# Optimization experiments

Measured on AMD Instinct MI355X. Metric: run time of the kernel, lower is better.

Reference implementation:

```python
import jax, jax.numpy as jnp
import numpy as np

N = 100000   # total nodes (batched graphs)
E = 800000   # random edges (self-loops appended -> E+N total)
G = 2000     # number of graphs in batch
H = 4        # heads per GAT layer
D = 64       # hidden_size (per-head out dim)
IN = 64      # in_feats
EXTRA = 8    # extra graph-level feats
HID = H * D  # 256


def setup_inputs() -> dict:
    key = jax.random.key(0)
    ks = jax.random.split(key, 24)
    s = 0.5  # init std used in the torch module
    feats_node = jax.random.normal(ks[0], (N, IN), jnp.float32)
    feats_graph = jax.random.normal(ks[1], (G, EXTRA), jnp.float32)
    # edges + self loops (DGL GATConv requires no zero-in-degree nodes)
    src = jnp.concatenate([jax.random.randint(ks[2], (E,), 0, N), jnp.arange(N)])
    dst = jnp.concatenate([jax.random.randint(ks[3], (E,), 0, N), jnp.arange(N)])
    node_gid = jnp.sort(jax.random.randint(ks[4], (N,), 0, G))
    # GAT layer 1
    W1 = jax.random.normal(ks[5], (IN, HID), jnp.float32) * s
    al1 = jax.random.normal(ks[6], (H, D), jnp.float32) * s
    ar1 = jax.random.normal(ks[7], (H, D), jnp.float32) * s
    b1 = jnp.zeros((HID,), jnp.float32)
    # GAT layer 2
    W2 = jax.random.normal(ks[8], (HID, HID), jnp.float32) * s
    al2 = jax.random.normal(ks[9], (H, D), jnp.float32) * s
    ar2 = jax.random.normal(ks[10], (H, D), jnp.float32) * s
    b2 = jnp.zeros((HID,), jnp.float32)
    # WeightedAverage readout score
    Ws = jax.random.normal(ks[11], (HID, 1), jnp.float32) * s
    bs = jnp.zeros((1,), jnp.float32)
    # MLP: 264 -> 128 -> 64 -> 1 with SELU
    Wm1 = jax.random.normal(ks[12], (HID + EXTRA, 2 * D), jnp.float32) * s
    bm1 = jnp.zeros((2 * D,), jnp.float32)
    Wm2 = jax.random.normal(ks[13], (2 * D, D), jnp.float32) * s
    bm2 = jnp.zeros((D,), jnp.float32)
    Wm3 = jax.random.normal(ks[14], (D, 1), jnp.float32) * s
    bm3 = jnp.zeros((1,), jnp.float32)
    return dict(feats_node=feats_node, feats_graph=feats_graph,
                W1=W1, al1=al1, ar1=ar1, b1=b1,
                W2=W2, al2=al2, ar2=ar2, b2=b2,
                Ws=Ws, bs=bs, Wm1=Wm1, bm1=bm1, Wm2=Wm2, bm2=bm2,
                Wm3=Wm3, bm3=bm3,
                src=src, dst=dst, node_gid=node_gid)


def gat_layer(x, W, al, ar, b, src, dst):
    # DGL GATConv: fc -> per-node attn projections -> edge leaky_relu ->
    # edge softmax over incoming edges -> weighted scatter-sum -> +bias
    f = (x @ W).reshape(N, H, D)                       # [N,H,D]
    el = jnp.einsum('nhd,hd->nh', f, al)               # [N,H]
    er = jnp.einsum('nhd,hd->nh', f, ar)               # [N,H]
    e = jax.nn.leaky_relu(el[src] + er[dst], 0.2)      # [E',H]
    m = jax.ops.segment_max(e, dst, num_segments=N)    # per-dst max
    e = jnp.exp(e - m[dst])
    denom = jax.ops.segment_sum(e, dst, num_segments=N)
    alpha = e / denom[dst]                             # edge softmax [E',H]
    out = jax.ops.segment_sum(alpha[:, :, None] * f[src], dst, num_segments=N)
    return out.reshape(N, HID) + b


def reference(feats_node, feats_graph, W1, al1, ar1, b1, W2, al2, ar2, b2,
              Ws, bs, Wm1, bm1, Wm2, bm2, Wm3, bm3, src, dst, node_gid):
    x = jax.nn.relu(gat_layer(feats_node, W1, al1, ar1, b1, src, dst))
    x = jax.nn.relu(gat_layer(x, W2, al2, ar2, b2, src, dst))
    # weighted-average readout per graph: sum(w*x)/sum(w)
    w = jax.nn.sigmoid(x @ Ws + bs)                    # [N,1]
    num = jax.ops.segment_sum(w * x, node_gid, num_segments=G)
    den = jax.ops.segment_sum(w, node_gid, num_segments=G)
    emb = num / jnp.where(den == 0, 1.0, den)          # [G,HID]
    h = jnp.concatenate([emb, feats_graph], axis=1)    # [G,HID+EXTRA]
    h = jax.nn.selu(h @ Wm1 + bm1)
    h = jax.nn.selu(h @ Wm2 + bm2)
    return h @ Wm3 + bm3                               # [G,1]
```

## Files before the change

kernel.cpp:

```cpp
#include <hip/hip_runtime.h>
#include <hip/hip_bf16.h>
#include <math.h>

#define NN     100000
#define GG     2000
#define HH     4
#define DD     64
#define HID    256
#define INF_   64
#define EXTRA  8

typedef unsigned short u16;
typedef __attribute__((ext_vector_type(8))) short bf16x8;
typedef __attribute__((ext_vector_type(4))) float f32x4;

__device__ __forceinline__ u16 f2bf(float f) {
    unsigned u = __float_as_uint(f);
    return (u16)((u + 0x7fffu + ((u >> 16) & 1u)) >> 16);
}
__device__ __forceinline__ float bf2f(u16 v) {
    return __uint_as_float(((unsigned)v) << 16);
}

__global__ __launch_bounds__(256) void wsplit_kernel(
    const float* __restrict__ W, u16* __restrict__ hi, u16* __restrict__ lo,
    int K, int lgK)
{
    int idx = blockIdx.x * 256 + threadIdx.x;
    if (idx >= 256 * K) return;
    int n = idx >> lgK, k = idx & (K - 1);
    float w = W[k * HID + n];
    u16 h = f2bf(w);
    hi[idx] = h;
    lo[idx] = f2bf(w - bf2f(h));
}

__global__ __launch_bounds__(256) void walprep_kernel(
    const float* __restrict__ W1, const float* __restrict__ al,
    const float* __restrict__ ar, float* __restrict__ wal, float* __restrict__ war)
{
    int tid = threadIdx.x;
    int d = tid >> 2, h = tid & 3;
    const float* wrow = W1 + d * HID + h * DD;
    const float* av = al + h * DD;
    const float* bv = ar + h * DD;
    float s1 = 0.f, s2 = 0.f;
    for (int c = 0; c < DD; ++c) { s1 += wrow[c] * av[c]; s2 += wrow[c] * bv[c]; }
    wal[d * 4 + h] = s1;
    war[d * 4 + h] = s2;
}

__global__ __launch_bounds__(256) void elr1_kernel(
    const float* __restrict__ feats, const float* __restrict__ wal,
    const float* __restrict__ war, float* __restrict__ el, float* __restrict__ er)
{
    int idx = blockIdx.x * 256 + threadIdx.x;
    if (idx >= NN * HH) return;
    int n = idx >> 2, h = idx & 3;
    const float* f = feats + (size_t)n * INF_;
    float s1 = 0.f, s2 = 0.f;
    #pragma unroll 4
    for (int d = 0; d < INF_; d += 4) {
        float4 fv = *reinterpret_cast<const float4*>(f + d);
        s1 += fv.x * wal[(d + 0) * 4 + h] + fv.y * wal[(d + 1) * 4 + h]
            + fv.z * wal[(d + 2) * 4 + h] + fv.w * wal[(d + 3) * 4 + h];
        s2 += fv.x * war[(d + 0) * 4 + h] + fv.y * war[(d + 1) * 4 + h]
            + fv.z * war[(d + 2) * 4 + h] + fv.w * war[(d + 3) * 4 + h];
    }
    el[idx] = s1;
    er[idx] = s2;
}

__global__ __launch_bounds__(256) void aggregate_feats_kernel(
    const float* __restrict__ feats, const float* __restrict__ w,
    const float* __restrict__ invden, const int* __restrict__ rowptr,
    const int* __restrict__ colsrc, u16* __restrict__ Yh, u16* __restrict__ Yl)
{
    int t = blockIdx.x * 4 + (threadIdx.x >> 6);
    int lane = threadIdx.x & 63;
    if (t >= NN) return;
    int beg = rowptr[t], end = rowptr[t + 1];
    float a0 = 0.f, a1 = 0.f, a2 = 0.f, a3 = 0.f;
    float b0 = 0.f, b1 = 0.f, b2 = 0.f, b3 = 0.f;
    int i = beg;
    for (; i + 1 < end; i += 2) {
        int s0 = colsrc[i], s1 = colsrc[i + 1];
        float4 w0 = *reinterpret_cast<const float4*>(w + (size_t)i * 4);
        float4 w1 = *reinterpret_cast<const float4*>(w + (size_t)(i + 1) * 4);
        float f0 = feats[(size_t)s0 * INF_ + lane];
        float f1 = feats[(size_t)s1 * INF_ + lane];
        a0 += w0.x * f0; a1 += w0.y * f0; a2 += w0.z * f0; a3 += w0.w * f0;
        b0 += w1.x * f1; b1 += w1.y * f1; b2 += w1.z * f1; b3 += w1.w * f1;
    }
    if (i < end) {
        int s0 = colsrc[i];
        float4 w0 = *reinterpret_cast<const float4*>(w + (size_t)i * 4);
        float f0 = feats[(size_t)s0 * INF_ + lane];
        a0 += w0.x * f0; a1 += w0.y * f0; a2 += w0.z * f0; a3 += w0.w * f0;
    }
    float4 inv = *reinterpret_cast<const float4*>(invden + (size_t)t * 4);
    float y0 = (a0 + b0) * inv.x;
    float y1 = (a1 + b1) * inv.y;
    float y2 = (a2 + b2) * inv.z;
    float y3 = (a3 + b3) * inv.w;
    u16* yh = Yh + (size_t)t * HID;
    u16* yl = Yl + (size_t)t * HID;
    u16 h0 = f2bf(y0), h1 = f2bf(y1), h2 = f2bf(y2), h3 = f2bf(y3);
    yh[lane] = h0;        yl[lane] = f2bf(y0 - bf2f(h0));
    yh[64 + lane] = h1;   yl[64 + lane] = f2bf(y1 - bf2f(h1));
    yh[128 + lane] = h2;  yl[128 + lane] = f2bf(y2 - bf2f(h2));
    yh[192 + lane] = h3;  yl[192 + lane] = f2bf(y3 - bf2f(h3));
}

__global__ __launch_bounds__(256) void gemm_head_kernel(
    const u16* __restrict__ Yh, const u16* __restrict__ Yl,
    const u16* __restrict__ BThi, const u16* __restrict__ BTlo,
    const float* __restrict__ bias,
    u16* __restrict__ Xh, u16* __restrict__ Xl, int M)
{
    __shared__ __align__(16) u16 Ah[128 * 64];
    __shared__ __align__(16) u16 Al[128 * 64];
    __shared__ __align__(16) u16 Bh[64 * 64];
    __shared__ __align__(16) u16 Bl[64 * 64];
    const int tid  = threadIdx.x;
    const int wave = tid >> 6, lane = tid & 63;
    const int quad = lane >> 4, l15 = lane & 15;
    const int wy = wave >> 1, wx = wave & 1;
    const int head = blockIdx.y;
    const int r0 = blockIdx.x * 128;
    const int cb = head * DD;

    {
        int row = tid >> 1, half = tid & 1;
        int gr = min(r0 + row, M - 1);
        size_t goff = (size_t)gr * HID + cb;
        #pragma unroll
        for (int m = 0; m < 4; ++m) {
            int c = half * 4 + m;
            int cs = c ^ (row & 7);
            *reinterpret_cast<bf16x8*>(&Ah[row * 64 + cs * 8]) =
                *reinterpret_cast<const bf16x8*>(Yh + goff + c * 8);
            *reinterpret_cast<bf16x8*>(&Al[row * 64 + cs * 8]) =
                *reinterpret_cast<const bf16x8*>(Yl + goff + c * 8);
        }
        int d = tid & 63, seg = tid >> 6;
        size_t boff = (size_t)(head * DD + d) * 64;
        #pragma unroll
        for (int m = 0; m < 2; ++m) {
            int c = seg * 2 + m;
            int cs = c ^ (d & 7);
            *reinterpret_cast<bf16x8*>(&Bh[d * 64 + cs * 8]) =
                *reinterpret_cast<const bf16x8*>(BThi + boff + c * 8);
            *reinterpret_cast<bf16x8*>(&Bl[d * 64 + cs * 8]) =
                *reinterpret_cast<const bf16x8*>(BTlo + boff + c * 8);
        }
    }
    __syncthreads();

    f32x4 acc[4][2];
    #pragma unroll
    for (int i = 0; i < 4; ++i)
        #pragma unroll
        for (int j = 0; j < 2; ++j)
            acc[i][j] = (f32x4){0.f, 0.f, 0.f, 0.f};

    #pragma unroll
    for (int k0 = 0; k0 < 64; k0 += 32) {
        bf16x8 afh[4], afl[4], bfh[2], bfl[2];
        #pragma unroll
        for (int i = 0; i < 4; ++i) {
            int Ra = wy * 64 + i * 16 + l15;
            int c = (k0 >> 3) + quad;
            int cs = c ^ (Ra & 7);
            afh[i] = *reinterpret_cast<const bf16x8*>(&Ah[Ra * 64 + cs * 8]);
            afl[i] = *reinterpret_cast<const bf16x8*>(&Al[Ra * 64 + cs * 8]);
        }
        #pragma unroll
        for (int j = 0; j < 2; ++j) {
            int Rb = wx * 32 + j * 16 + l15;
            int c = (k0 >> 3) + quad;
            int cs = c ^ (Rb & 7);
            bfh[j] = *reinterpret_cast<const bf16x8*>(&Bh[Rb * 64 + cs * 8]);
            bfl[j] = *reinterpret_cast<const bf16x8*>(&Bl[Rb * 64 + cs * 8]);
        }
        #pragma unroll
        for (int i = 0; i < 4; ++i)
            #pragma unroll
            for (int j = 0; j < 2; ++j) {
                acc[i][j] = __builtin_amdgcn_mfma_f32_16x16x32_bf16(afh[i], bfh[j], acc[i][j], 0, 0, 0);
                acc[i][j] = __builtin_amdgcn_mfma_f32_16x16x32_bf16(afl[i], bfh[j], acc[i][j], 0, 0, 0);
                acc[i][j] = __builtin_amdgcn_mfma_f32_16x16x32_bf16(afh[i], bfl[j], acc[i][j], 0, 0, 0);
            }
    }

    float bv[2];
    #pragma unroll
    for (int j = 0; j < 2; ++j) bv[j] = bias[cb + wx * 32 + j * 16 + l15];
    #pragma unroll
    for (int i = 0; i < 4; ++i)
        #pragma unroll
        for (int rr = 0; rr < 4; ++rr) {
            int grow = r0 + wy * 64 + i * 16 + quad * 4 + rr;
            if (grow < M) {
                size_t base = (size_t)grow * HID + cb + wx * 32 + l15;
                #pragma unroll
                for (int j = 0; j < 2; ++j) {
                    float x = fmaxf(acc[i][j][rr] + bv[j], 0.f);
                    u16 h = f2bf(x);
                    Xh[base + j * 16] = h;
                    Xl[base + j * 16] = f2bf(x - bf2f(h));
                }
            }
        }
}

__global__ __launch_bounds__(256) void mfma_gemm_kernel(
    const u16* __restrict__ Ahg, const u16* __restrict__ Alg,
    const u16* __restrict__ BThi, const u16* __restrict__ BTlo,
    u16* __restrict__ Cb,
    const float* __restrict__ al, const float* __restrict__ ar,
    float* __restrict__ el, float* __restrict__ er, int M, int K)
{
    __shared__ __align__(16) u16 Ah[128 * 32];
    __shared__ __align__(16) u16 Al[128 * 32];
    __shared__ __align__(16) u16 Bh[128 * 32];
    __shared__ __align__(16) u16 Bl[128 * 32];
    const int tid  = threadIdx.x;
    const int wave = tid >> 6, lane = tid & 63;
    const int quad = lane >> 4, l15 = lane & 15;
    const int wy = wave >> 1, wx = wave & 1;
    const int r0 = blockIdx.x * 128, c0 = blockIdx.y * 128;
    const int sr = tid >> 2, sseg = tid & 3;

    f32x4 acc[4][4];
    #pragma unroll
    for (int i = 0; i < 4; ++i)
        #pragma unroll
        for (int j = 0; j < 4; ++j)
            acc[i][j] = (f32x4){0.f, 0.f, 0.f, 0.f};

    for (int k0 = 0; k0 < K; k0 += 32) {
        #pragma unroll
        for (int half = 0; half < 2; ++half) {
            int r = sr + half * 64;
            int cs = (sseg ^ (r & 3)) * 8;
            int gr = min(r0 + r, M - 1);
            size_t aoff = (size_t)gr * K + k0 + sseg * 8;
            *reinterpret_cast<bf16x8*>(&Ah[r * 32 + cs]) =
                *reinterpret_cast<const bf16x8*>(Ahg + aoff);
            *reinterpret_cast<bf16x8*>(&Al[r * 32 + cs]) =
                *reinterpret_cast<const bf16x8*>(Alg + aoff);
            int gc = c0 + r;
            size_t boff = (size_t)gc * K + k0 + sseg * 8;
            *reinterpret_cast<bf16x8*>(&Bh[r * 32 + cs]) =
                *reinterpret_cast<const bf16x8*>(BThi + boff);
            *reinterpret_cast<bf16x8*>(&Bl[r * 32 + cs]) =
                *reinterpret_cast<const bf16x8*>(BTlo + boff);
        }
        __syncthreads();
        bf16x8 afh[4], afl[4], bfh[4], bfl[4];
        #pragma unroll
        for (int i = 0; i < 4; ++i) {
            int Ra = wy * 64 + i * 16 + l15;
            int off = Ra * 32 + (quad ^ (Ra & 3)) * 8;
            afh[i] = *reinterpret_cast<const bf16x8*>(&Ah[off]);
            afl[i] = *reinterpret_cast<const bf16x8*>(&Al[off]);
        }
        #pragma unroll
        for (int j = 0; j < 4; ++j) {
            int Rb = wx * 64 + j * 16 + l15;
            int off = Rb * 32 + (quad ^ (Rb & 3)) * 8;
            bfh[j] = *reinterpret_cast<const bf16x8*>(&Bh[off]);
            bfl[j] = *reinterpret_cast<const bf16x8*>(&Bl[off]);
        }
        #pragma unroll
        for (int i = 0; i < 4; ++i)
            #pragma unroll
            for (int j = 0; j < 4; ++j) {
                acc[i][j] = __builtin_amdgcn_mfma_f32_16x16x32_bf16(afh[i], bfh[j], acc[i][j], 0, 0, 0);
                acc[i][j] = __builtin_amdgcn_mfma_f32_16x16x32_bf16(afl[i], bfh[j], acc[i][j], 0, 0, 0);
                acc[i][j] = __builtin_amdgcn_mfma_f32_16x16x32_bf16(afh[i], bfl[j], acc[i][j], 0, 0, 0);
            }
        __syncthreads();
    }

    #pragma unroll
    for (int i = 0; i < 4; ++i)
        #pragma unroll
        for (int rr = 0; rr < 4; ++rr) {
            int grow = r0 + wy * 64 + i * 16 + quad * 4 + rr;
            if (grow < M) {
                u16* crow = Cb + (size_t)grow * HID + c0 + wx * 64 + l15;
                #pragma unroll
                for (int j = 0; j < 4; ++j) crow[j * 16] = f2bf(acc[i][j][rr]);
            }
        }

    const int h = blockIdx.y * 2 + wx;
    float alf[4], arf[4];
    #pragma unroll
    for (int j = 0; j < 4; ++j) {
        alf[j] = al[h * DD + j * 16 + l15];
        arf[j] = ar[h * DD + j * 16 + l15];
    }
    #pragma unroll
    for (int i = 0; i < 4; ++i)
        #pragma unroll
        for (int rr = 0; rr < 4; ++rr) {
            float sl = acc[i][0][rr] * alf[0] + acc[i][1][rr] * alf[1]
                     + acc[i][2][rr] * alf[2] + acc[i][3][rr] * alf[3];
            float sr_ = acc[i][0][rr] * arf[0] + acc[i][1][rr] * arf[1]
                      + acc[i][2][rr] * arf[2] + acc[i][3][rr] * arf[3];
            #pragma unroll
            for (int off = 1; off < 16; off <<= 1) {
                sl  += __shfl_xor(sl, off, 64);
                sr_ += __shfl_xor(sr_, off, 64);
            }
            if (l15 == 0) {
                int grow = r0 + wy * 64 + i * 16 + quad * 4 + rr;
                if (grow < M) {
                    el[grow * 4 + h] = sl;
                    er[grow * 4 + h] = sr_;
                }
            }
        }
}

__device__ __forceinline__ float leaky02(float x) { return x > 0.f ? x : 0.2f * x; }

__global__ __launch_bounds__(256) void edge_softmax_kernel(
    const float* __restrict__ el, const float* __restrict__ er,
    const int* __restrict__ rowptr, const int* __restrict__ colsrc,
    float* __restrict__ w, float* __restrict__ invden)
{
    int idx = blockIdx.x * 256 + threadIdx.x;
    if (idx >= NN * HH) return;
    int t = idx >> 2, h = idx & 3;
    int beg = rowptr[t], end = rowptr[t + 1];
    float ert = er[idx];
    float m = -1e30f;
    for (int i = beg; i < end; ++i) {
        int s = colsrc[i];
        m = fmaxf(m, leaky02(el[s * 4 + h] + ert));
    }
    float den = 0.f;
    for (int i = beg; i < end; ++i) {
        int s = colsrc[i];
        float v = expf(leaky02(el[s * 4 + h] + ert) - m);
        w[(size_t)i * 4 + h] = v;
        den += v;
    }
    invden[idx] = 1.f / den;
}

__global__ __launch_bounds__(256) void aggregate_bf16_kernel(
    const u16* __restrict__ F, const float* __restrict__ w,
    const float* __restrict__ invden, const int* __restrict__ rowptr,
    const int* __restrict__ colsrc, const float* __restrict__ bias,
    u16* __restrict__ out)
{
    int t = blockIdx.x * 4 + (threadIdx.x >> 6);
    int lane = threadIdx.x & 63;
    if (t >= NN) return;
    int beg = rowptr[t], end = rowptr[t + 1];
    const int h = lane >> 4;
    float4 acc0 = make_float4(0.f, 0.f, 0.f, 0.f);
    float4 acc1 = make_float4(0.f, 0.f, 0.f, 0.f);
    int i = beg;
    for (; i + 1 < end; i += 2) {
        int s0 = colsrc[i], s1 = colsrc[i + 1];
        float w0 = w[(size_t)i * 4 + h];
        float w1 = w[(size_t)(i + 1) * 4 + h];
        ushort4 f0 = *reinterpret_cast<const ushort4*>(F + (size_t)s0 * HID + 4 * lane);
        ushort4 f1 = *reinterpret_cast<const ushort4*>(F + (size_t)s1 * HID + 4 * lane);
        acc0.x += w0 * bf2f(f0.x); acc0.y += w0 * bf2f(f0.y);
        acc0.z += w0 * bf2f(f0.z); acc0.w += w0 * bf2f(f0.w);
        acc1.x += w1 * bf2f(f1.x); acc1.y += w1 * bf2f(f1.y);
        acc1.z += w1 * bf2f(f1.z); acc1.w += w1 * bf2f(f1.w);
    }
    if (i < end) {
        int s0 = colsrc[i];
        float w0 = w[(size_t)i * 4 + h];
        ushort4 f0 = *reinterpret_cast<const ushort4*>(F + (size_t)s0 * HID + 4 * lane);
        acc0.x += w0 * bf2f(f0.x); acc0.y += w0 * bf2f(f0.y);
        acc0.z += w0 * bf2f(f0.z); acc0.w += w0 * bf2f(f0.w);
    }
    float inv = invden[t * 4 + h];
    float4 bv = *reinterpret_cast<const float4*>(bias + 4 * lane);
    ushort4 r;
    r.x = f2bf(fmaxf((acc0.x + acc1.x) * inv + bv.x, 0.f));
    r.y = f2bf(fmaxf((acc0.y + acc1.y) * inv + bv.y, 0.f));
    r.z = f2bf(fmaxf((acc0.z + acc1.z) * inv + bv.z, 0.f));
    r.w = f2bf(fmaxf((acc0.w + acc1.w) * inv + bv.w, 0.f));
    *reinterpret_cast<ushort4*>(out + (size_t)t * HID + 4 * lane) = r;
}

__global__ __launch_bounds__(256) void readout_kernel(
    const u16* __restrict__ X, const float* __restrict__ Ws,
    const float* __restrict__ bs, const int* __restrict__ gptr,
    float* __restrict__ emb)
{
    int g = blockIdx.x * 4 + (threadIdx.x >> 6);
    int lane = threadIdx.x & 63;
    if (g >= GG) return;
    int beg = gptr[g], end = gptr[g + 1];
    float4 wv = *reinterpret_cast<const float4*>(Ws + 4 * lane);
    float b = bs[0];
    float4 acc = make_float4(0.f, 0.f, 0.f, 0.f);
    float wsum = 0.f;
    for (int n = beg; n < end; ++n) {
        ushort4 xv = *reinterpret_cast<const ushort4*>(X + (size_t)n * HID + 4 * lane);
        float x0 = bf2f(xv.x), x1 = bf2f(xv.y), x2 = bf2f(xv.z), x3 = bf2f(xv.w);
        float p = x0 * wv.x + x1 * wv.y + x2 * wv.z + x3 * wv.w;
        #pragma unroll
        for (int off = 32; off; off >>= 1) p += __shfl_xor(p, off, 64);
        float w = 1.f / (1.f + expf(-(p + b)));
        wsum += w;
        acc.x += w * x0; acc.y += w * x1; acc.z += w * x2; acc.w += w * x3;
    }
    float inv = (wsum == 0.f) ? 1.f : wsum;
    float4 e;
    e.x = acc.x / inv; e.y = acc.y / inv; e.z = acc.z / inv; e.w = acc.w / inv;
    *reinterpret_cast<float4*>(emb + (size_t)g * HID + 4 * lane) = e;
}

__device__ __forceinline__ float selu_f(float x)
{
    const float scale = 1.0507009873554805f, alpha = 1.6732632423543772f;
    return scale * (x > 0.f ? x : alpha * expm1f(x));
}

__global__ __launch_bounds__(128) void mlp_kernel(
    const float* __restrict__ emb, const float* __restrict__ fg,
    const float* __restrict__ Wm1, const float* __restrict__ bm1,
    const float* __restrict__ Wm2, const float* __restrict__ bm2,
    const float* __restrict__ Wm3, const float* __restrict__ bm3,
    float* __restrict__ out)
{
    int g = blockIdx.x;
    __shared__ float h[HID + EXTRA];
    __shared__ float h1[128];
    __shared__ float h2[64];
    int tid = threadIdx.x;
    h[tid] = emb[(size_t)g * HID + tid];
    h[128 + tid] = emb[(size_t)g * HID + 128 + tid];
    if (tid < EXTRA) h[HID + tid] = fg[(size_t)g * EXTRA + tid];
    __syncthreads();
    float acc = bm1[tid];
    for (int i = 0; i < HID + EXTRA; ++i) acc += h[i] * Wm1[i * 128 + tid];
    h1[tid] = selu_f(acc);
    __syncthreads();
    if (tid < 64) {
        float acc2 = bm2[tid];
        for (int i = 0; i < 128; ++i) acc2 += h1[i] * Wm2[i * 64 + tid];
        h2[tid] = selu_f(acc2);
    }
    __syncthreads();
    if (tid < 64) {
        float p = h2[tid] * Wm3[tid];
        #pragma unroll
        for (int off = 32; off; off >>= 1) p += __shfl_xor(p, off, 64);
        if (tid == 0) out[g] = p + bm3[0];
    }
}

__global__ void count_dst_kernel(const int* __restrict__ dst, int* __restrict__ cnt, int E)
{
    int e = blockIdx.x * 256 + threadIdx.x;
    if (e < E) atomicAdd(&cnt[dst[e]], 1);
}
__global__ void count_gid_kernel(const int* __restrict__ gid, int* __restrict__ cnt, int n)
{
    int i = blockIdx.x * 256 + threadIdx.x;
    if (i < n) atomicAdd(&cnt[gid[i]], 1);
}
__global__ void fill_csr_kernel(const int* __restrict__ src, const int* __restrict__ dst,
                                int* __restrict__ cursor, int* __restrict__ colsrc, int E)
{
    int e = blockIdx.x * 256 + threadIdx.x;
    if (e < E) {
        int p = atomicAdd(&cursor[dst[e]], 1);
        colsrc[p] = src[e];
    }
}

__global__ __launch_bounds__(256) void scan_blocks_kernel(
    const int* __restrict__ in, int n, int* __restrict__ out, int* __restrict__ partials)
{
    __shared__ int lds[256];
    int tid = threadIdx.x;
    int base = blockIdx.x * 1024 + tid * 4;
    int v0 = (base + 0 < n) ? in[base + 0] : 0;
    int v1 = (base + 1 < n) ? in[base + 1] : 0;
    int v2 = (base + 2 < n) ? in[base + 2] : 0;
    int v3 = (base + 3 < n) ? in[base + 3] : 0;
    int s = v0 + v1 + v2 + v3;
    lds[tid] = s;
    __syncthreads();
    for (int off = 1; off < 256; off <<= 1) {
        int t = (tid >= off) ? lds[tid - off] : 0;
        __syncthreads();
        lds[tid] += t;
        __syncthreads();
    }
    int excl = lds[tid] - s;
    if (base + 0 < n) out[base + 0] = excl;
    if (base + 1 < n) out[base + 1] = excl + v0;
    if (base + 2 < n) out[base + 2] = excl + v0 + v1;
    if (base + 3 < n) out[base + 3] = excl + v0 + v1 + v2;
    if (tid == 255) partials[blockIdx.x] = lds[255];
}

__global__ __launch_bounds__(256) void scan_partials_kernel(int* partials, int nb)
{
    __shared__ int lds[256];
    int tid = threadIdx.x;
    int v = (tid < nb) ? partials[tid] : 0;
    lds[tid] = v;
    __syncthreads();
    for (int off = 1; off < 256; off <<= 1) {
        int t = (tid >= off) ? lds[tid - off] : 0;
        __syncthreads();
        lds[tid] += t;
        __syncthreads();
    }
    int excl = lds[tid] - v;
    if (tid < nb) partials[tid] = excl;
}

__global__ void add_offsets_kernel(int* __restrict__ out, const int* __restrict__ partials, int n)
{
    int i = blockIdx.x * 256 + threadIdx.x;
    if (i < n) out[i] += partials[i >> 10];
}

extern "C" void kernel_launch(void* const* d_in, const int* in_sizes, int n_in,
                              void* d_out, int out_size, void* d_ws, size_t ws_size,
                              hipStream_t stream)
{
    const float* feats_node  = (const float*)d_in[0];
    const float* feats_graph = (const float*)d_in[1];
    const float* W1  = (const float*)d_in[2];
    const float* al1 = (const float*)d_in[3];
    const float* ar1 = (const float*)d_in[4];
    const float* b1  = (const float*)d_in[5];
    const float* W2  = (const float*)d_in[6];
    const float* al2 = (const float*)d_in[7];
    const float* ar2 = (const float*)d_in[8];
    const float* b2  = (const float*)d_in[9];
    const float* Ws  = (const float*)d_in[10];
    const float* bs  = (const float*)d_in[11];
    const float* Wm1 = (const float*)d_in[12];
    const float* bm1 = (const float*)d_in[13];
    const float* Wm2 = (const float*)d_in[14];
    const float* bm2 = (const float*)d_in[15];
    const float* Wm3 = (const float*)d_in[16];
    const float* bm3 = (const float*)d_in[17];
    const int* src = (const int*)d_in[18];
    const int* dst = (const int*)d_in[19];
    const int* gid = (const int*)d_in[20];
    float* out = (float*)d_out;
    const int E = in_sizes[18];

    char* p = (char*)d_ws;
    auto alloc = [&](size_t bytes) {
        char* r = p;
        p += (bytes + 255) & ~(size_t)255;
        return r;
    };
    u16*   Yh     = (u16*)alloc((size_t)NN * HID * 2);
    u16*   Yl     = (u16*)alloc((size_t)NN * HID * 2);
    u16*   Xh     = (u16*)alloc((size_t)NN * HID * 2);
    u16*   Xl     = (u16*)alloc((size_t)NN * HID * 2);
    float* el     = (float*)alloc((size_t)NN * HH * 4);
    float* er     = (float*)alloc((size_t)NN * HH * 4);
    float* wbuf   = (float*)alloc((size_t)E * HH * 4);
    float* invden = (float*)alloc((size_t)NN * HH * 4);
    int*   cnt    = (int*)alloc((size_t)(NN + 1) * 4);
    int*   rowptr = (int*)alloc((size_t)(NN + 1) * 4);
    int*   colsrc = (int*)alloc((size_t)E * 4);
    int*   gcnt   = (int*)alloc((size_t)(GG + 1) * 4);
    int*   gptr   = (int*)alloc((size_t)(GG + 1) * 4);
    int*   parts  = (int*)alloc(1024 * 4);
    float* emb    = (float*)alloc((size_t)GG * HID * 4);
    u16*   BT1h   = (u16*)alloc((size_t)HID * INF_ * 2);
    u16*   BT1l   = (u16*)alloc((size_t)HID * INF_ * 2);
    u16*   BT2h   = (u16*)alloc((size_t)HID * HID * 2);
    u16*   BT2l   = (u16*)alloc((size_t)HID * HID * 2);
    float* wal1   = (float*)alloc(INF_ * HH * 4);
    float* war1   = (float*)alloc(INF_ * HH * 4);
    u16*   Fbf2   = Yh;
    u16*   Xbf2   = Xh;

    hipMemsetAsync(cnt, 0, (size_t)(NN + 1) * 4, stream);
    count_dst_kernel<<<(E + 255) / 256, 256, 0, stream>>>(dst, cnt, E);
    {
        int n = NN + 1, nb = (n + 1023) / 1024;
        scan_blocks_kernel<<<nb, 256, 0, stream>>>(cnt, n, rowptr, parts);
        scan_partials_kernel<<<1, 256, 0, stream>>>(parts, nb);
        add_offsets_kernel<<<(n + 255) / 256, 256, 0, stream>>>(rowptr, parts, n);
    }
    hipMemcpyAsync(cnt, rowptr, (size_t)(NN + 1) * 4, hipMemcpyDeviceToDevice, stream);
    fill_csr_kernel<<<(E + 255) / 256, 256, 0, stream>>>(src, dst, cnt, colsrc, E);

    hipMemsetAsync(gcnt, 0, (size_t)(GG + 1) * 4, stream);
    count_gid_kernel<<<(NN + 255) / 256, 256, 0, stream>>>(gid, gcnt, NN);
    {
        int n = GG + 1, nb = (n + 1023) / 1024;
        scan_blocks_kernel<<<nb, 256, 0, stream>>>(gcnt, n, gptr, parts);
        scan_partials_kernel<<<1, 256, 0, stream>>>(parts, nb);
        add_offsets_kernel<<<(n + 255) / 256, 256, 0, stream>>>(gptr, parts, n);
    }

    wsplit_kernel<<<(HID * INF_ + 255) / 256, 256, 0, stream>>>(W1, BT1h, BT1l, INF_, 6);
    wsplit_kernel<<<(HID * HID + 255) / 256, 256, 0, stream>>>(W2, BT2h, BT2l, HID, 8);
    walprep_kernel<<<1, 256, 0, stream>>>(W1, al1, ar1, wal1, war1);

    const int nh_blocks = (NN * HH + 255) / 256;

    elr1_kernel<<<nh_blocks, 256, 0, stream>>>(feats_node, wal1, war1, el, er);
    edge_softmax_kernel<<<nh_blocks, 256, 0, stream>>>(el, er, rowptr, colsrc, wbuf, invden);
    aggregate_feats_kernel<<<(NN + 3) / 4, 256, 0, stream>>>(feats_node, wbuf, invden,
                                                             rowptr, colsrc, Yh, Yl);
    {
        dim3 hgrid((NN + 127) / 128, HH);
        gemm_head_kernel<<<hgrid, 256, 0, stream>>>(Yh, Yl, BT1h, BT1l, b1, Xh, Xl, NN);
    }

    dim3 ggrid((NN + 127) / 128, HID / 128);
    mfma_gemm_kernel<<<ggrid, 256, 0, stream>>>(
        Xh, Xl, BT2h, BT2l, Fbf2, al2, ar2, el, er, NN, HID);
    edge_softmax_kernel<<<nh_blocks, 256, 0, stream>>>(el, er, rowptr, colsrc, wbuf, invden);
    aggregate_bf16_kernel<<<(NN + 3) / 4, 256, 0, stream>>>(Fbf2, wbuf, invden, rowptr, colsrc,
                                                            b2, Xbf2);

    readout_kernel<<<(GG + 3) / 4, 256, 0, stream>>>(Xbf2, Ws, bs, gptr, emb);
    mlp_kernel<<<GG, 128, 0, stream>>>(emb, feats_graph, Wm1, bm1, Wm2, bm2, Wm3, bm3, out);
}
```

Measured before the change: 630.5 us.

## Fuse layer-2 edge softmax into aggregation, fix LDS swizzle, compute graph ranges directly

Layer-2 edge softmax now runs inside the aggregation kernel, which recomputes the max, exponentials and denominator per node. This removes one kernel launch and the round-trip of per-edge weights through global memory, at the cost of redundant exp work across lanes and an extra pass over the edges for the max. The GEMM LDS swizzle now XORs with (row>>1)&3 to reduce bank conflicts. Graph pointer ranges are computed directly from the sorted gid array instead of atomic counting plus a multi-kernel scan.

```diff
diff --git a/kernel.cpp b/kernel.cpp
--- a/kernel.cpp
+++ b/kernel.cpp
@@ -69,6 +69,33 @@
     }
     el[idx] = s1;
     er[idx] = s2;
+}
+
+__device__ __forceinline__ float leaky02(float x) { return x > 0.f ? x : 0.2f * x; }
+
+__global__ __launch_bounds__(256) void edge_softmax_kernel(
+    const float* __restrict__ el, const float* __restrict__ er,
+    const int* __restrict__ rowptr, const int* __restrict__ colsrc,
+    float* __restrict__ w, float* __restrict__ invden)
+{
+    int idx = blockIdx.x * 256 + threadIdx.x;
+    if (idx >= NN * HH) return;
+    int t = idx >> 2, h = idx & 3;
+    int beg = rowptr[t], end = rowptr[t + 1];
+    float ert = er[idx];
+    float m = -1e30f;
+    for (int i = beg; i < end; ++i) {
+        int s = colsrc[i];
+        m = fmaxf(m, leaky02(el[s * 4 + h] + ert));
+    }
+    float den = 0.f;
+    for (int i = beg; i < end; ++i) {
+        int s = colsrc[i];
+        float v = expf(leaky02(el[s * 4 + h] + ert) - m);
+        w[(size_t)i * 4 + h] = v;
+        den += v;
+    }
+    invden[idx] = 1.f / den;
 }
 
 __global__ __launch_bounds__(256) void aggregate_feats_kernel(
@@ -243,7 +270,7 @@
         #pragma unroll
         for (int half = 0; half < 2; ++half) {
             int r = sr + half * 64;
-            int cs = (sseg ^ (r & 3)) * 8;
+            int cs = (sseg ^ ((r >> 1) & 3)) * 8;
             int gr = min(r0 + r, M - 1);
             size_t aoff = (size_t)gr * K + k0 + sseg * 8;
             *reinterpret_cast<bf16x8*>(&Ah[r * 32 + cs]) =
@@ -262,14 +289,14 @@
         #pragma unroll
         for (int i = 0; i < 4; ++i) {
             int Ra = wy * 64 + i * 16 + l15;
-            int off = Ra * 32 + (quad ^ (Ra & 3)) * 8;
+            int off = Ra * 32 + (quad ^ ((Ra >> 1) & 3)) * 8;
             afh[i] = *reinterpret_cast<const bf16x8*>(&Ah[off]);
             afl[i] = *reinterpret_cast<const bf16x8*>(&Al[off]);
         }
         #pragma unroll
         for (int j = 0; j < 4; ++j) {
             int Rb = wx * 64 + j * 16 + l15;
-            int off = Rb * 32 + (quad ^ (Rb & 3)) * 8;
+            int off = Rb * 32 + (quad ^ ((Rb >> 1) & 3)) * 8;
             bfh[j] = *reinterpret_cast<const bf16x8*>(&Bh[off]);
             bfl[j] = *reinterpret_cast<const bf16x8*>(&Bl[off]);
         }
@@ -326,36 +353,9 @@
         }
 }
 
-__device__ __forceinline__ float leaky02(float x) { return x > 0.f ? x : 0.2f * x; }
-
-__global__ __launch_bounds__(256) void edge_softmax_kernel(
-    const float* __restrict__ el, const float* __restrict__ er,
-    const int* __restrict__ rowptr, const int* __restrict__ colsrc,
-    float* __restrict__ w, float* __restrict__ invden)
-{
-    int idx = blockIdx.x * 256 + threadIdx.x;
-    if (idx >= NN * HH) return;
-    int t = idx >> 2, h = idx & 3;
-    int beg = rowptr[t], end = rowptr[t + 1];
-    float ert = er[idx];
-    float m = -1e30f;
-    for (int i = beg; i < end; ++i) {
-        int s = colsrc[i];
-        m = fmaxf(m, leaky02(el[s * 4 + h] + ert));
-    }
-    float den = 0.f;
-    for (int i = beg; i < end; ++i) {
-        int s = colsrc[i];
-        float v = expf(leaky02(el[s * 4 + h] + ert) - m);
-        w[(size_t)i * 4 + h] = v;
-        den += v;
-    }
-    invden[idx] = 1.f / den;
-}
-
 __global__ __launch_bounds__(256) void aggregate_bf16_kernel(
-    const u16* __restrict__ F, const float* __restrict__ w,
-    const float* __restrict__ invden, const int* __restrict__ rowptr,
+    const u16* __restrict__ F, const float* __restrict__ el,
+    const float* __restrict__ er, const int* __restrict__ rowptr,
     const int* __restrict__ colsrc, const float* __restrict__ bias,
     u16* __restrict__ out)
 {
@@ -364,13 +364,19 @@
     if (t >= NN) return;
     int beg = rowptr[t], end = rowptr[t + 1];
     const int h = lane >> 4;
+    float ert = er[t * 4 + h];
+    float m = -1e30f;
+    for (int i = beg; i < end; ++i)
+        m = fmaxf(m, leaky02(el[colsrc[i] * 4 + h] + ert));
+    float den = 0.f;
     float4 acc0 = make_float4(0.f, 0.f, 0.f, 0.f);
     float4 acc1 = make_float4(0.f, 0.f, 0.f, 0.f);
     int i = beg;
     for (; i + 1 < end; i += 2) {
         int s0 = colsrc[i], s1 = colsrc[i + 1];
-        float w0 = w[(size_t)i * 4 + h];
-        float w1 = w[(size_t)(i + 1) * 4 + h];
+        float w0 = expf(leaky02(el[s0 * 4 + h] + ert) - m);
+        float w1 = expf(leaky02(el[s1 * 4 + h] + ert) - m);
+        den += w0; den += w1;
         ushort4 f0 = *reinterpret_cast<const ushort4*>(F + (size_t)s0 * HID + 4 * lane);
         ushort4 f1 = *reinterpret_cast<const ushort4*>(F + (size_t)s1 * HID + 4 * lane);
         acc0.x += w0 * bf2f(f0.x); acc0.y += w0 * bf2f(f0.y);
@@ -380,12 +386,13 @@
     }
     if (i < end) {
         int s0 = colsrc[i];
-        float w0 = w[(size_t)i * 4 + h];
+        float w0 = expf(leaky02(el[s0 * 4 + h] + ert) - m);
+        den += w0;
         ushort4 f0 = *reinterpret_cast<const ushort4*>(F + (size_t)s0 * HID + 4 * lane);
         acc0.x += w0 * bf2f(f0.x); acc0.y += w0 * bf2f(f0.y);
         acc0.z += w0 * bf2f(f0.z); acc0.w += w0 * bf2f(f0.w);
     }
-    float inv = invden[t * 4 + h];
+    float inv = 1.f / den;
     float4 bv = *reinterpret_cast<const float4*>(bias + 4 * lane);
     ushort4 r;
     r.x = f2bf(fmaxf((acc0.x + acc1.x) * inv + bv.x, 0.f));
@@ -469,11 +476,6 @@
     int e = blockIdx.x * 256 + threadIdx.x;
     if (e < E) atomicAdd(&cnt[dst[e]], 1);
 }
-__global__ void count_gid_kernel(const int* __restrict__ gid, int* __restrict__ cnt, int n)
-{
-    int i = blockIdx.x * 256 + threadIdx.x;
-    if (i < n) atomicAdd(&cnt[gid[i]], 1);
-}
 __global__ void fill_csr_kernel(const int* __restrict__ src, const int* __restrict__ dst,
                                 int* __restrict__ cursor, int* __restrict__ colsrc, int E)
 {
@@ -482,6 +484,17 @@
         int p = atomicAdd(&cursor[dst[e]], 1);
         colsrc[p] = src[e];
     }
+}
+
+__global__ void gid_ranges_kernel(const int* __restrict__ gid, int* __restrict__ gptr, int n)
+{
+    int i = blockIdx.x * 256 + threadIdx.x;
+    if (i >= n) return;
+    int cur = gid[i];
+    int prev = (i == 0) ? -1 : gid[i - 1];
+    for (int g = prev + 1; g <= cur; ++g) gptr[g] = i;
+    if (i == n - 1)
+        for (int g = cur + 1; g <= GG; ++g) gptr[g] = n;
 }
 
 __global__ __launch_bounds__(256) void scan_blocks_kernel(
@@ -579,7 +592,6 @@
     int*   cnt    = (int*)alloc((size_t)(NN + 1) * 4);
     int*   rowptr = (int*)alloc((size_t)(NN + 1) * 4);
     int*   colsrc = (int*)alloc((size_t)E * 4);
-    int*   gcnt   = (int*)alloc((size_t)(GG + 1) * 4);
     int*   gptr   = (int*)alloc((size_t)(GG + 1) * 4);
     int*   parts  = (int*)alloc(1024 * 4);
     float* emb    = (float*)alloc((size_t)GG * HID * 4);
@@ -603,14 +615,7 @@
     hipMemcpyAsync(cnt, rowptr, (size_t)(NN + 1) * 4, hipMemcpyDeviceToDevice, stream);
     fill_csr_kernel<<<(E + 255) / 256, 256, 0, stream>>>(src, dst, cnt, colsrc, E);
 
-    hipMemsetAsync(gcnt, 0, (size_t)(GG + 1) * 4, stream);
-    count_gid_kernel<<<(NN + 255) / 256, 256, 0, stream>>>(gid, gcnt, NN);
-    {
-        int n = GG + 1, nb = (n + 1023) / 1024;
-        scan_blocks_kernel<<<nb, 256, 0, stream>>>(gcnt, n, gptr, parts);
-        scan_partials_kernel<<<1, 256, 0, stream>>>(parts, nb);
-        add_offsets_kernel<<<(n + 255) / 256, 256, 0, stream>>>(gptr, parts, n);
-    }
+    gid_ranges_kernel<<<(NN + 255) / 256, 256, 0, stream>>>(gid, gptr, NN);
 
     wsplit_kernel<<<(HID * INF_ + 255) / 256, 256, 0, stream>>>(W1, BT1h, BT1l, INF_, 6);
     wsplit_kernel<<<(HID * HID + 255) / 256, 256, 0, stream>>>(W2, BT2h, BT2l, HID, 8);
@@ -630,8 +635,7 @@
     dim3 ggrid((NN + 127) / 128, HID / 128);
     mfma_gemm_kernel<<<ggrid, 256, 0, stream>>>(
         Xh, Xl, BT2h, BT2l, Fbf2, al2, ar2, el, er, NN, HID);
-    edge_softmax_kernel<<<nh_blocks, 256, 0, stream>>>(el, er, rowptr, colsrc, wbuf, invden);
-    aggregate_bf16_kernel<<<(NN + 3) / 4, 256, 0, stream>>>(Fbf2, wbuf, invden, rowptr, colsrc,
+    aggregate_bf16_kernel<<<(NN + 3) / 4, 256, 0, stream>>>(Fbf2, el, er, rowptr, colsrc,
                                                             b2, Xbf2);
 
     readout_kernel<<<(GG + 3) / 4, 256, 0, stream>>>(Xbf2, Ws, bs, gptr, emb);
```

Result: no change. 626.4 us (-0.7%).
